# Optimization experiments

Hardware: AMD Instinct MI355X
Metric: run time of the kernel (lower is better)

Reference implementation:

```python
import jax, jax.numpy as jnp
import numpy as np

NUM_HEADS = 16
DIM = 1024

def setup_inputs() -> dict:
    key = jax.random.key(0)
    ks = jax.random.split(key, 12)
    B, N, T, C = 4, 4096, 77, DIM
    s = 1.0 / np.sqrt(C)
    return {
        "hidden_states": jax.random.normal(ks[0], (B, N, C), jnp.float32),
        "encoder_hidden_states": jax.random.normal(ks[1], (B, T, C), jnp.float32),
        "attention_mask": jnp.zeros((B, N, T), jnp.float32),
        "Wq": jax.random.normal(ks[2], (C, C), jnp.float32) * s,
        "bq": jnp.zeros((C,), jnp.float32),
        "Wk": jax.random.normal(ks[3], (C, C), jnp.float32) * s,
        "bk": jnp.zeros((C,), jnp.float32),
        "Wv": jax.random.normal(ks[4], (C, C), jnp.float32) * s,
        "bv": jnp.zeros((C,), jnp.float32),
        "Wo": jax.random.normal(ks[5], (C, C), jnp.float32) * s,
        "bo": jnp.zeros((C,), jnp.float32),
    }

def reference(hidden_states, encoder_hidden_states, attention_mask,
              Wq, bq, Wk, bk, Wv, bv, Wo, bo):
    B, N, C = hidden_states.shape
    T = encoder_hidden_states.shape[1]
    H = NUM_HEADS
    D = C // H
    # QKV projections (torch Linear: x @ W.T + b)
    q = (hidden_states @ Wq.T + bq).reshape(B, N, H, D).transpose(0, 2, 1, 3)   # bhnd
    k = (encoder_hidden_states @ Wk.T + bk).reshape(B, T, H, D).transpose(0, 2, 1, 3)  # bhtd
    v = (encoder_hidden_states @ Wv.T + bv).reshape(B, T, H, D).transpose(0, 2, 1, 3)  # bhtd
    scale = 1.0 / jnp.sqrt(jnp.asarray(D, q.dtype))
    # scores [B,H,N,T]; additive mask broadcast over heads
    scores = jnp.einsum('bhnd,bhtd->bhnt', q, k) * scale + attention_mask[:, None, :, :]
    attn = jax.nn.softmax(scores, axis=-1)
    out = jnp.einsum('bhnt,bhtd->bhnd', attn, v)
    out = out.transpose(0, 2, 1, 3).reshape(B, N, C)
    return out @ Wo.T + bo
```

## Files before the change

### kernel.cpp

```cpp
#include <hip/hip_runtime.h>
#include <cstdint>

typedef __bf16 bf16x8 __attribute__((ext_vector_type(8)));
typedef float f32x4 __attribute__((ext_vector_type(4)));
typedef unsigned short u16;
typedef unsigned int u32;

__device__ __forceinline__ u16 f2bf(float f) {
    u32 u = __builtin_bit_cast(u32, f);
    u += 0x7fffu + ((u >> 16) & 1u);
    return (u16)(u >> 16);
}

__device__ __forceinline__ void gl_lds16(const u16* g, u16* l) {
    __builtin_amdgcn_global_load_lds(
        (const __attribute__((address_space(1))) void*)g,
        (__attribute__((address_space(3))) void*)l,
        16, 0, 0);
}

__device__ __forceinline__ f32x4 mfma16(bf16x8 a, bf16x8 b, f32x4 c) {
    return __builtin_amdgcn_mfma_f32_16x16x32_bf16(a, b, c, 0, 0, 0);
}


__global__ void cvt_pad(const float* __restrict__ src, u16* __restrict__ dst,
                        int srcn, int totn) {
    int i = (blockIdx.x * 256 + threadIdx.x) * 4;
    if (i >= totn) return;
    float4 v = make_float4(0.f, 0.f, 0.f, 0.f);
    if (i < srcn) v = *(const float4*)&src[i];
    ushort4 o;
    o.x = f2bf(v.x); o.y = f2bf(v.y); o.z = f2bf(v.z); o.w = f2bf(v.w);
    *(ushort4*)&dst[i] = o;
}

struct CvtArgs {
    const float* s[5];
    u16* d[5];
    int srcn[5];
    int totn[5];
};

__global__ void cvt_multi(CvtArgs a) {
    const int seg = blockIdx.y;
    int i = (blockIdx.x * 256 + threadIdx.x) * 4;
    if (i >= a.totn[seg]) return;
    float4 v = make_float4(0.f, 0.f, 0.f, 0.f);
    if (i < a.srcn[seg]) v = *(const float4*)&a.s[seg][i];
    ushort4 o;
    o.x = f2bf(v.x); o.y = f2bf(v.y); o.z = f2bf(v.z); o.w = f2bf(v.w);
    *(ushort4*)&a.d[seg][i] = o;
}

__device__ __forceinline__ void store_out(u16* C, long idx, float v) { C[idx] = f2bf(v); }
__device__ __forceinline__ void store_out(float* C, long idx, float v) { C[idx] = v; }

template <typename OutT, bool BA, bool BC>
__global__ __launch_bounds__(512, 2) void gemm8p(
    const u16* __restrict__ A, const u16* __restrict__ W,
    const float* __restrict__ bias, OutT* __restrict__ C,
    int M, int N, int K) {
    __shared__ __align__(16) u16 As[2][256 * 64];
    __shared__ __align__(16) u16 Bs[2][256 * 64];

    const int tid = threadIdx.x;
    const int wid = tid >> 6, l = tid & 63;
    const int wr = wid >> 2, wc = wid & 3;
    const int l15 = l & 15, lg = l >> 4;

    const int lin = blockIdx.y * gridDim.x + blockIdx.x;
    const int cpx = (gridDim.x * gridDim.y) >> 3;
    const int swz = (lin & 7) * cpx + (lin >> 3);
    const long tn = swz % gridDim.x;
    const long tm = swz / gridDim.x;

    const int srow = tid >> 3;
    const int schunk = (tid & 7) ^ (srow & 7);

    long aBase, aQ, aT;
    if (BA) {
        const long rq = tm * 256 + srow;
        aBase = ((long)(schunk >> 1) * (M >> 2) + (rq >> 2)) * 64 +
                (srow & 3) * 16 + (schunk & 1) * 8;
        aQ = 1024;
        aT = 64L * M;
    } else {
        aBase = (tm * 256 + srow) * (long)K + schunk * 8;
        aQ = 64L * K;
        aT = 64;
    }
    const long bBase = (tn * 256 + srow) * (long)K + schunk * 8;

    const int rxor = l15 & 7;
    const int rdo0 = ((0 * 4 + lg) ^ rxor) * 8;
    const int rdo1 = ((1 * 4 + lg) ^ rxor) * 8;

    const int NT = K >> 6;

#define STAGE_A(bufi, q_, t_)                                                 \
    gl_lds16(A + aBase + (q_)*aQ + (long)(t_)*aT, &As[bufi][(q_)*4096 + tid * 8])
#define STAGE_B(bufi, q_, t_)                                                 \
    gl_lds16(W + bBase + (long)(q_)*64 * K + (long)(t_)*64,                   \
             &Bs[bufi][(q_)*4096 + tid * 8])

    f32x4 acc[8][4] = {};

#pragma unroll
    for (int q = 0; q < 4; ++q) { STAGE_A(0, q, 0); STAGE_B(0, q, 0); }
#pragma unroll
    for (int q = 0; q < 4; ++q) STAGE_B(1, q, 1);
    STAGE_A(1, 0, 1); STAGE_A(1, 2, 1);
    asm volatile("s_waitcnt vmcnt(6)" ::: "memory");
    __builtin_amdgcn_sched_barrier(0);
    __builtin_amdgcn_s_barrier();

    const int arow = wr * 128 + l15;
    const int brow = wc * 64 + l15;

    for (int t = 0; t < NT; ++t) {
        const int c = t & 1;
        const u16* __restrict__ Ap = &As[c][0];
        const u16* __restrict__ Bp = &Bs[c][0];
        const bool s1 = (t + 1) < NT;
        const bool s2 = (t + 2) < NT;
        bf16x8 b[4][2];

        {
            bf16x8 a[2][2];
#pragma unroll
            for (int mi = 0; mi < 2; ++mi) {
                a[mi][0] = *(const bf16x8*)&Ap[(arow + mi * 16) * 64 + rdo0];
                a[mi][1] = *(const bf16x8*)&Ap[(arow + mi * 16) * 64 + rdo1];
            }
#pragma unroll
            for (int nf = 0; nf < 4; ++nf) {
                b[nf][0] = *(const bf16x8*)&Bp[(brow + nf * 16) * 64 + rdo0];
                b[nf][1] = *(const bf16x8*)&Bp[(brow + nf * 16) * 64 + rdo1];
            }
            if (s1) STAGE_A(c ^ 1, 1, t + 1);
            __builtin_amdgcn_s_barrier();
            asm volatile("s_waitcnt lgkmcnt(0)" ::: "memory");
            __builtin_amdgcn_sched_barrier(0);
            __builtin_amdgcn_s_setprio(1);
#pragma unroll
            for (int mi = 0; mi < 2; ++mi)
#pragma unroll
                for (int nf = 0; nf < 4; ++nf) {
                    acc[mi][nf] = mfma16(a[mi][0], b[nf][0], acc[mi][nf]);
                    acc[mi][nf] = mfma16(a[mi][1], b[nf][1], acc[mi][nf]);
                }
            __builtin_amdgcn_s_setprio(0);
            __builtin_amdgcn_s_barrier();
        }
        {
            bf16x8 a[2][2];
#pragma unroll
            for (int mi = 0; mi < 2; ++mi) {
                a[mi][0] = *(const bf16x8*)&Ap[(arow + (mi + 2) * 16) * 64 + rdo0];
                a[mi][1] = *(const bf16x8*)&Ap[(arow + (mi + 2) * 16) * 64 + rdo1];
            }
            if (s1) STAGE_A(c ^ 1, 3, t + 1);
            if (s2) { STAGE_B(c, 0, t + 2); STAGE_B(c, 1, t + 2); }
            __builtin_amdgcn_s_barrier();
            asm volatile("s_waitcnt lgkmcnt(0)" ::: "memory");
            __builtin_amdgcn_sched_barrier(0);
            __builtin_amdgcn_s_setprio(1);
#pragma unroll
            for (int mi = 0; mi < 2; ++mi)
#pragma unroll
                for (int nf = 0; nf < 4; ++nf) {
                    acc[mi + 2][nf] = mfma16(a[mi][0], b[nf][0], acc[mi + 2][nf]);
                    acc[mi + 2][nf] = mfma16(a[mi][1], b[nf][1], acc[mi + 2][nf]);
                }
            __builtin_amdgcn_s_setprio(0);
            __builtin_amdgcn_s_barrier();
        }
        {
            bf16x8 a[2][2];
#pragma unroll
            for (int mi = 0; mi < 2; ++mi) {
                a[mi][0] = *(const bf16x8*)&Ap[(arow + (mi + 4) * 16) * 64 + rdo0];
                a[mi][1] = *(const bf16x8*)&Ap[(arow + (mi + 4) * 16) * 64 + rdo1];
            }
            if (s2) { STAGE_B(c, 2, t + 2); STAGE_B(c, 3, t + 2); STAGE_A(c, 0, t + 2); }
            __builtin_amdgcn_s_barrier();
            asm volatile("s_waitcnt lgkmcnt(0)" ::: "memory");
            __builtin_amdgcn_sched_barrier(0);
            __builtin_amdgcn_s_setprio(1);
#pragma unroll
            for (int mi = 0; mi < 2; ++mi)
#pragma unroll
                for (int nf = 0; nf < 4; ++nf) {
                    acc[mi + 4][nf] = mfma16(a[mi][0], b[nf][0], acc[mi + 4][nf]);
                    acc[mi + 4][nf] = mfma16(a[mi][1], b[nf][1], acc[mi + 4][nf]);
                }
            __builtin_amdgcn_s_setprio(0);
            __builtin_amdgcn_s_barrier();
        }
        {
            bf16x8 a[2][2];
#pragma unroll
            for (int mi = 0; mi < 2; ++mi) {
                a[mi][0] = *(const bf16x8*)&Ap[(arow + (mi + 6) * 16) * 64 + rdo0];
                a[mi][1] = *(const bf16x8*)&Ap[(arow + (mi + 6) * 16) * 64 + rdo1];
            }
            if (s2) STAGE_A(c, 2, t + 2);
            __builtin_amdgcn_s_barrier();
            asm volatile("s_waitcnt lgkmcnt(0)" ::: "memory");
            __builtin_amdgcn_sched_barrier(0);
            __builtin_amdgcn_s_setprio(1);
#pragma unroll
            for (int mi = 0; mi < 2; ++mi)
#pragma unroll
                for (int nf = 0; nf < 4; ++nf) {
                    acc[mi + 6][nf] = mfma16(a[mi][0], b[nf][0], acc[mi + 6][nf]);
                    acc[mi + 6][nf] = mfma16(a[mi][1], b[nf][1], acc[mi + 6][nf]);
                }
            __builtin_amdgcn_s_setprio(0);
            if (s2)
                asm volatile("s_waitcnt vmcnt(6)" ::: "memory");
            else
                asm volatile("s_waitcnt vmcnt(0)" ::: "memory");
            __builtin_amdgcn_sched_barrier(0);
            __builtin_amdgcn_s_barrier();
        }
    }
#undef STAGE_A
#undef STAGE_B

    const long row0 = tm * 256 + wr * 128;
    const long col0 = tn * 256 + wc * 64;
    float bv[4];
#pragma unroll
    for (int nf = 0; nf < 4; ++nf) bv[nf] = bias[col0 + nf * 16 + l15];
    if (BC) {
        const long ct0 = col0 >> 4;
        const long rb = row0 >> 2;
#pragma unroll
        for (int mf = 0; mf < 8; ++mf)
#pragma unroll
            for (int nf = 0; nf < 4; ++nf)
#pragma unroll
                for (int r = 0; r < 4; ++r) {
                    const long idx =
                        ((ct0 + nf) * (long)(M >> 2) + rb + mf * 4 + lg) * 64 +
                        r * 16 + l15;
                    store_out(C, idx, acc[mf][nf][r] + bv[nf]);
                }
    } else {
#pragma unroll
        for (int mf = 0; mf < 8; ++mf)
#pragma unroll
            for (int nf = 0; nf < 4; ++nf)
#pragma unroll
                for (int r = 0; r < 4; ++r) {
                    const long row = row0 + mf * 16 + lg * 4 + r;
                    const long col = col0 + nf * 16 + l15;
                    store_out(C, row * N + col, acc[mf][nf][r] + bv[nf]);
                }
    }
}

template <bool VT>
__device__ __forceinline__ void gemm128_body(
    const u16* __restrict__ A, const u16* __restrict__ W,
    const float* __restrict__ bias, u16* __restrict__ C,
    int N, int K) {
    __shared__ u16 As[128 * 64];
    __shared__ u16 Bs[128 * 64];
    const int tid = threadIdx.x;
    const int w = tid >> 6, l = tid & 63;
    const int wr = w >> 1, wc = w & 1;
    const int l15 = l & 15, lg = l >> 4;
    const long tm = blockIdx.y, tn = blockIdx.x;
    const u16* Ab = A + tm * 128 * (long)K;
    const u16* Bb = W + tn * 128 * (long)K;

    f32x4 acc[4][4] = {};

    for (int k0 = 0; k0 < K; k0 += 64) {
#pragma unroll
        for (int t = 0; t < 4; ++t) {
            int i = t * 256 + tid;
            int row = i >> 3, cc = i & 7;
            gl_lds16(Ab + (long)row * K + k0 + cc * 8, &As[i * 8]);
            gl_lds16(Bb + (long)row * K + k0 + cc * 8, &Bs[i * 8]);
        }
        __syncthreads();
#pragma unroll
        for (int kk = 0; kk < 64; kk += 32) {
            bf16x8 a[4], b[4];
#pragma unroll
            for (int m = 0; m < 4; ++m)
                a[m] = *(const bf16x8*)&As[(wr * 64 + m * 16 + l15) * 64 + kk + lg * 8];
#pragma unroll
            for (int n = 0; n < 4; ++n)
                b[n] = *(const bf16x8*)&Bs[(wc * 64 + n * 16 + l15) * 64 + kk + lg * 8];
#pragma unroll
            for (int m = 0; m < 4; ++m)
#pragma unroll
                for (int n = 0; n < 4; ++n)
                    acc[m][n] = mfma16(a[m], b[n], acc[m][n]);
        }
        __syncthreads();
    }

    const long row0 = tm * 128 + wr * 64;
    const long col0 = tn * 128 + wc * 64;
#pragma unroll
    for (int m = 0; m < 4; ++m)
#pragma unroll
        for (int n = 0; n < 4; ++n)
#pragma unroll
            for (int r = 0; r < 4; ++r) {
                const float v = acc[m][n][r] + bias[col0 + n * 16 + l15];
                if (VT) {
                    const int row = (int)(row0 + m * 16 + lg * 4 + r);
                    if (row < 308) {
                        const int bb = row / 77;
                        const int t = row - bb * 77;
                        const int ch = (int)(col0 + n * 16 + l15);
                        const long idx = (long)bb * 98304 +
                                         ((long)(t >> 4) * 256 + (ch >> 2)) * 64 +
                                         (ch & 3) * 16 + (t & 15);
                        C[idx] = f2bf(v);
                    }
                } else {
                    const long idx = (((col0 >> 4) + n) * 96L + (row0 >> 2) + m * 4 + lg) * 64 +
                                     r * 16 + l15;
                    C[idx] = f2bf(v);
                }
            }
}

__global__ __launch_bounds__(256) void gemm_kv(
    const u16* __restrict__ A,
    const u16* __restrict__ Wk, const float* __restrict__ bk, u16* __restrict__ Ko,
    const u16* __restrict__ Wv, const float* __restrict__ bv, u16* __restrict__ Vo,
    int N, int K) {
    if (blockIdx.z == 0)
        gemm128_body<false>(A, Wk, bk, Ko, N, K);
    else
        gemm128_body<true>(A, Wv, bv, Vo, N, K);
}

__global__ __launch_bounds__(256, 4) void attn_fused(
    const u16* __restrict__ Q,
    const u16* __restrict__ Kb,
    const u16* __restrict__ Vt,
    const float* __restrict__ mask,
    u16* __restrict__ Ao) {
    __shared__ u16 Ps[128 * 104];

    const int h = blockIdx.x, b = blockIdx.y, nt = blockIdx.z;
    const int tid = threadIdx.x;
    const int w = tid >> 6, l = tid & 63;
    const int l15 = l & 15, lg = l >> 4;

    const int qrow = b * 4096 + nt * 128 + w * 32;

    f32x4 acc[6][2] = {};
#pragma unroll
    for (int kk = 0; kk < 64; kk += 32) {
        const int d = kk + lg * 8;
        const int cb = h * 4 + (d >> 4);
        const int dlow = d & 15;
        bf16x8 kf[6], qf[2];
#pragma unroll
        for (int n = 0; n < 6; ++n) {
            const int row = b * 77 + n * 16 + l15;
            kf[n] = *(const bf16x8*)&Kb[((long)cb * 96 + (row >> 2)) * 64 +
                                        (row & 3) * 16 + dlow];
        }
#pragma unroll
        for (int m = 0; m < 2; ++m) {
            const int row = qrow + m * 16 + l15;
            qf[m] = *(const bf16x8*)&Q[((long)cb * 4096 + (row >> 2)) * 64 +
                                       (row & 3) * 16 + dlow];
        }
#pragma unroll
        for (int n = 0; n < 6; ++n)
#pragma unroll
            for (int m = 0; m < 2; ++m)
                acc[n][m] = mfma16(kf[n], qf[m], acc[n][m]);
    }

    const float* mrow0 = mask + ((long)b * 4096 + nt * 128 + w * 32) * 77;
#pragma unroll
    for (int m = 0; m < 2; ++m) {
        const float* mrow = mrow0 + (m * 16 + l15) * 77;
        float vals[6][4];
        float rmax = -3e38f;
#pragma unroll
        for (int n = 0; n < 6; ++n) {
            const int t0 = n * 16 + lg * 4;
#pragma unroll
            for (int r = 0; r < 4; ++r) {
                const int t = t0 + r;
                float v = -3e38f;
                if (t < 77) v = acc[n][m][r] * 0.125f + mrow[t];
                vals[n][r] = v;
                rmax = fmaxf(rmax, v);
            }
        }
        rmax = fmaxf(rmax, __shfl_xor(rmax, 16, 64));
        rmax = fmaxf(rmax, __shfl_xor(rmax, 32, 64));
        float s = 0.f;
#pragma unroll
        for (int n = 0; n < 6; ++n)
#pragma unroll
            for (int r = 0; r < 4; ++r) {
                float e = (vals[n][r] > -1e37f) ? __expf(vals[n][r] - rmax) : 0.f;
                vals[n][r] = e;
                s += e;
            }
        s += __shfl_xor(s, 16, 64);
        s += __shfl_xor(s, 32, 64);
        const float inv = 1.f / s;
#pragma unroll
        for (int n = 0; n < 6; ++n) {
            const u32 lo = (u32)f2bf(vals[n][0] * inv) |
                           ((u32)f2bf(vals[n][1] * inv) << 16);
            const u32 hi = (u32)f2bf(vals[n][2] * inv) |
                           ((u32)f2bf(vals[n][3] * inv) << 16);
            *(uint2*)&Ps[(w * 32 + m * 16 + l15) * 104 + n * 16 + lg * 4] =
                make_uint2(lo, hi);
        }
    }

    f32x4 o[2][4] = {};
#pragma unroll
    for (int kt = 0; kt < 96; kt += 32) {
        bf16x8 pa[2], vf[4];
#pragma unroll
        for (int m = 0; m < 2; ++m)
            pa[m] = *(const bf16x8*)&Ps[(w * 32 + m * 16 + l15) * 104 + kt + lg * 8];
        const int t0 = kt + lg * 8;
#pragma unroll
        for (int n = 0; n < 4; ++n) {
            const int ch = h * 64 + n * 16 + l15;
            vf[n] = *(const bf16x8*)&Vt[(long)b * 98304 +
                                        ((long)(t0 >> 4) * 256 + (ch >> 2)) * 64 +
                                        (ch & 3) * 16 + (t0 & 15)];
        }
#pragma unroll
        for (int m = 0; m < 2; ++m)
#pragma unroll
            for (int n = 0; n < 4; ++n)
                o[m][n] = mfma16(pa[m], vf[n], o[m][n]);
    }

#pragma unroll
    for (int m = 0; m < 2; ++m)
#pragma unroll
        for (int n = 0; n < 4; ++n)
#pragma unroll
            for (int r = 0; r < 4; ++r) {
                const long idx = ((long)(h * 4 + n) * 4096 +
                                  b * 1024 + nt * 32 + w * 8 + m * 4 + lg) * 64 +
                                 r * 16 + l15;
                Ao[idx] = f2bf(o[m][n][r]);
            }
}

extern "C" void kernel_launch(void* const* d_in, const int* in_sizes, int n_in,
                              void* d_out, int out_size, void* d_ws, size_t ws_size,
                              hipStream_t stream) {
    const float* hidden = (const float*)d_in[0];
    const float* enc = (const float*)d_in[1];
    const float* mask = (const float*)d_in[2];
    const float* Wq = (const float*)d_in[3];
    const float* bq = (const float*)d_in[4];
    const float* Wk = (const float*)d_in[5];
    const float* bk = (const float*)d_in[6];
    const float* Wv = (const float*)d_in[7];
    const float* bv = (const float*)d_in[8];
    const float* Wo = (const float*)d_in[9];
    const float* bo = (const float*)d_in[10];
    float* out = (float*)d_out;

    char* ws = (char*)d_ws;
    u16* hiddenB = (u16*)(ws);
    u16* Qb = (u16*)(ws + 33554432L);
    u16* AoB = (u16*)(ws + 2 * 33554432L);
    u16* WqB = (u16*)(ws + 3 * 33554432L);
    u16* WkB = WqB + 1048576;
    u16* WvB = WkB + 1048576;
    u16* WoB = WvB + 1048576;
    u16* encB = WoB + 1048576;
    u16* Kbuf = encB + 393216;
    u16* VtBuf = Kbuf + 393216;

    cvt_pad<<<dim3(16384), 256, 0, stream>>>(hidden, hiddenB, 16777216, 16777216);
    CvtArgs ca;
    ca.s[0] = Wq;  ca.d[0] = WqB; ca.srcn[0] = 1048576; ca.totn[0] = 1048576;
    ca.s[1] = Wk;  ca.d[1] = WkB; ca.srcn[1] = 1048576; ca.totn[1] = 1048576;
    ca.s[2] = Wv;  ca.d[2] = WvB; ca.srcn[2] = 1048576; ca.totn[2] = 1048576;
    ca.s[3] = Wo;  ca.d[3] = WoB; ca.srcn[3] = 1048576; ca.totn[3] = 1048576;
    ca.s[4] = enc; ca.d[4] = encB; ca.srcn[4] = 315392; ca.totn[4] = 393216;
    cvt_multi<<<dim3(1024, 5), 256, 0, stream>>>(ca);

    gemm8p<u16, false, true><<<dim3(4, 64), 512, 0, stream>>>(
        hiddenB, WqB, bq, Qb, 16384, 1024, 1024);
    gemm_kv<<<dim3(8, 3, 2), 256, 0, stream>>>(encB, WkB, bk, Kbuf, WvB, bv, VtBuf, 1024, 1024);

    attn_fused<<<dim3(16, 4, 32), 256, 0, stream>>>(Qb, Kbuf, VtBuf, mask, AoB);

    gemm8p<float, true, false><<<dim3(4, 64), 512, 0, stream>>>(
        AoB, WoB, bo, out, 16384, 1024, 1024);
}
```

Measured before the change: 166.5 us.

## Shrink GEMM tiles to 256x128 with simpler double buffering, merge conversions, trim attention tiles

Replaces the 256x256, K=64 GEMM with a 256x128, K=32 tile. It uses a plain double-buffered loop with one barrier per step, doubling the block count to 512 and cutting LDS use. The two fp32-to-bf16 conversion launches become a single launch that maps block ranges to segments. Attention now computes 5 key tiles instead of 6, masks padded keys with a large negative value instead of a branch, and zero-fills the pad region of the P buffer. The risks are more global traffic per FLOP and lost fine-grained overlap in the GEMM.

```diff
diff --git a/kernel.cpp b/kernel.cpp
--- a/kernel.cpp
+++ b/kernel.cpp
@@ -24,27 +24,20 @@
 }
 
 
-__global__ void cvt_pad(const float* __restrict__ src, u16* __restrict__ dst,
-                        int srcn, int totn) {
-    int i = (blockIdx.x * 256 + threadIdx.x) * 4;
-    if (i >= totn) return;
-    float4 v = make_float4(0.f, 0.f, 0.f, 0.f);
-    if (i < srcn) v = *(const float4*)&src[i];
-    ushort4 o;
-    o.x = f2bf(v.x); o.y = f2bf(v.y); o.z = f2bf(v.z); o.w = f2bf(v.w);
-    *(ushort4*)&dst[i] = o;
-}
-
-struct CvtArgs {
-    const float* s[5];
-    u16* d[5];
-    int srcn[5];
-    int totn[5];
+struct CvtAll {
+    const float* s[6];
+    u16* d[6];
+    int srcn[6];
+    int totn[6];
+    int off[6];
 };
 
-__global__ void cvt_multi(CvtArgs a) {
-    const int seg = blockIdx.y;
-    int i = (blockIdx.x * 256 + threadIdx.x) * 4;
+__global__ void cvt_all(CvtAll a) {
+    const int blk = blockIdx.x;
+    int seg = 0;
+#pragma unroll
+    for (int s = 1; s < 6; ++s) seg += (blk >= a.off[s]);
+    const int i = ((blk - a.off[seg]) * 256 + threadIdx.x) * 4;
     if (i >= a.totn[seg]) return;
     float4 v = make_float4(0.f, 0.f, 0.f, 0.f);
     if (i < a.srcn[seg]) v = *(const float4*)&a.s[seg][i];
@@ -57,180 +50,91 @@
 __device__ __forceinline__ void store_out(float* C, long idx, float v) { C[idx] = v; }
 
 template <typename OutT, bool BA, bool BC>
-__global__ __launch_bounds__(512, 2) void gemm8p(
+__global__ __launch_bounds__(512, 2) void gemmP(
     const u16* __restrict__ A, const u16* __restrict__ W,
     const float* __restrict__ bias, OutT* __restrict__ C,
     int M, int N, int K) {
-    __shared__ __align__(16) u16 As[2][256 * 64];
-    __shared__ __align__(16) u16 Bs[2][256 * 64];
+    __shared__ __align__(16) u16 As[2][256 * 32];
+    __shared__ __align__(16) u16 Bs[2][128 * 32];
 
     const int tid = threadIdx.x;
     const int wid = tid >> 6, l = tid & 63;
-    const int wr = wid >> 2, wc = wid & 3;
+    const int wr = wid >> 1, wc = wid & 1;
     const int l15 = l & 15, lg = l >> 4;
 
     const int lin = blockIdx.y * gridDim.x + blockIdx.x;
     const int cpx = (gridDim.x * gridDim.y) >> 3;
     const int swz = (lin & 7) * cpx + (lin >> 3);
-    const long tn = swz % gridDim.x;
-    const long tm = swz / gridDim.x;
-
-    const int srow = tid >> 3;
-    const int schunk = (tid & 7) ^ (srow & 7);
-
-    long aBase, aQ, aT;
-    if (BA) {
-        const long rq = tm * 256 + srow;
-        aBase = ((long)(schunk >> 1) * (M >> 2) + (rq >> 2)) * 64 +
-                (srow & 3) * 16 + (schunk & 1) * 8;
-        aQ = 1024;
-        aT = 64L * M;
-    } else {
-        aBase = (tm * 256 + srow) * (long)K + schunk * 8;
-        aQ = 64L * K;
-        aT = 64;
-    }
-    const long bBase = (tn * 256 + srow) * (long)K + schunk * 8;
-
-    const int rxor = l15 & 7;
-    const int rdo0 = ((0 * 4 + lg) ^ rxor) * 8;
-    const int rdo1 = ((1 * 4 + lg) ^ rxor) * 8;
-
-    const int NT = K >> 6;
-
-#define STAGE_A(bufi, q_, t_)                                                 \
-    gl_lds16(A + aBase + (q_)*aQ + (long)(t_)*aT, &As[bufi][(q_)*4096 + tid * 8])
-#define STAGE_B(bufi, q_, t_)                                                 \
-    gl_lds16(W + bBase + (long)(q_)*64 * K + (long)(t_)*64,                   \
-             &Bs[bufi][(q_)*4096 + tid * 8])
-
-    f32x4 acc[8][4] = {};
-
-#pragma unroll
-    for (int q = 0; q < 4; ++q) { STAGE_A(0, q, 0); STAGE_B(0, q, 0); }
-#pragma unroll
-    for (int q = 0; q < 4; ++q) STAGE_B(1, q, 1);
-    STAGE_A(1, 0, 1); STAGE_A(1, 2, 1);
-    asm volatile("s_waitcnt vmcnt(6)" ::: "memory");
-    __builtin_amdgcn_sched_barrier(0);
-    __builtin_amdgcn_s_barrier();
-
-    const int arow = wr * 128 + l15;
-    const int brow = wc * 64 + l15;
+    const long tn = swz & 7;
+    const long tm = swz >> 3;
+
+    const int srp = tid >> 3;
+    const int sv = (tid & 7) ^ (srp & 7);
+    const int sE = (sv >> 2) & 1;
+    const int sKC = sv & 3;
+    const long ar0 = tm * 256 + 2 * srp + sE;
+    const long brow = tn * 128 + 2 * srp + sE;
+    const long aRB = ar0 >> 2;
+    const int aSub = (int)(ar0 & 3) * 16 + (sKC & 1) * 8;
+    const int aCB = sKC >> 1;
+
+    const int NT = K >> 5;
+
+#define STAGE(bufi, t_)                                                        \
+    do {                                                                       \
+        if (BA) {                                                              \
+            const long cb_ = (long)((t_) * 2 + aCB) * (M >> 2);                \
+            gl_lds16(A + (cb_ + aRB) * 64 + aSub, &As[bufi][tid * 8]);         \
+            gl_lds16(A + (cb_ + aRB + 32) * 64 + aSub,                         \
+                     &As[bufi][4096 + tid * 8]);                               \
+        } else {                                                               \
+            gl_lds16(A + ar0 * (long)K + (t_) * 32 + sKC * 8,                  \
+                     &As[bufi][tid * 8]);                                      \
+            gl_lds16(A + (ar0 + 128) * (long)K + (t_) * 32 + sKC * 8,          \
+                     &As[bufi][4096 + tid * 8]);                               \
+        }                                                                      \
+        gl_lds16(W + brow * (long)K + (t_) * 32 + sKC * 8,                     \
+                 &Bs[bufi][tid * 8]);                                          \
+    } while (0)
+
+    const int e = l15 & 1;
+    const int rphA = wr * 32 + (l15 >> 1);
+    const int rphB = wc * 32 + (l15 >> 1);
+    const int pA = ((e * 4 + lg) ^ (rphA & 7)) * 8;
+    const int pB = ((e * 4 + lg) ^ (rphB & 7)) * 8;
+    const int aOff = rphA * 64 + pA;
+    const int bOff = rphB * 64 + pB;
+
+    f32x4 acc[4][4] = {};
+
+    STAGE(0, 0);
+    __syncthreads();
 
     for (int t = 0; t < NT; ++t) {
         const int c = t & 1;
-        const u16* __restrict__ Ap = &As[c][0];
-        const u16* __restrict__ Bp = &Bs[c][0];
-        const bool s1 = (t + 1) < NT;
-        const bool s2 = (t + 2) < NT;
-        bf16x8 b[4][2];
-
-        {
-            bf16x8 a[2][2];
-#pragma unroll
-            for (int mi = 0; mi < 2; ++mi) {
-                a[mi][0] = *(const bf16x8*)&Ap[(arow + mi * 16) * 64 + rdo0];
-                a[mi][1] = *(const bf16x8*)&Ap[(arow + mi * 16) * 64 + rdo1];
-            }
-#pragma unroll
-            for (int nf = 0; nf < 4; ++nf) {
-                b[nf][0] = *(const bf16x8*)&Bp[(brow + nf * 16) * 64 + rdo0];
-                b[nf][1] = *(const bf16x8*)&Bp[(brow + nf * 16) * 64 + rdo1];
-            }
-            if (s1) STAGE_A(c ^ 1, 1, t + 1);
-            __builtin_amdgcn_s_barrier();
-            asm volatile("s_waitcnt lgkmcnt(0)" ::: "memory");
-            __builtin_amdgcn_sched_barrier(0);
-            __builtin_amdgcn_s_setprio(1);
-#pragma unroll
-            for (int mi = 0; mi < 2; ++mi)
-#pragma unroll
-                for (int nf = 0; nf < 4; ++nf) {
-                    acc[mi][nf] = mfma16(a[mi][0], b[nf][0], acc[mi][nf]);
-                    acc[mi][nf] = mfma16(a[mi][1], b[nf][1], acc[mi][nf]);
-                }
-            __builtin_amdgcn_s_setprio(0);
-            __builtin_amdgcn_s_barrier();
-        }
-        {
-            bf16x8 a[2][2];
-#pragma unroll
-            for (int mi = 0; mi < 2; ++mi) {
-                a[mi][0] = *(const bf16x8*)&Ap[(arow + (mi + 2) * 16) * 64 + rdo0];
-                a[mi][1] = *(const bf16x8*)&Ap[(arow + (mi + 2) * 16) * 64 + rdo1];
-            }
-            if (s1) STAGE_A(c ^ 1, 3, t + 1);
-            if (s2) { STAGE_B(c, 0, t + 2); STAGE_B(c, 1, t + 2); }
-            __builtin_amdgcn_s_barrier();
-            asm volatile("s_waitcnt lgkmcnt(0)" ::: "memory");
-            __builtin_amdgcn_sched_barrier(0);
-            __builtin_amdgcn_s_setprio(1);
-#pragma unroll
-            for (int mi = 0; mi < 2; ++mi)
-#pragma unroll
-                for (int nf = 0; nf < 4; ++nf) {
-                    acc[mi + 2][nf] = mfma16(a[mi][0], b[nf][0], acc[mi + 2][nf]);
-                    acc[mi + 2][nf] = mfma16(a[mi][1], b[nf][1], acc[mi + 2][nf]);
-                }
-            __builtin_amdgcn_s_setprio(0);
-            __builtin_amdgcn_s_barrier();
-        }
-        {
-            bf16x8 a[2][2];
-#pragma unroll
-            for (int mi = 0; mi < 2; ++mi) {
-                a[mi][0] = *(const bf16x8*)&Ap[(arow + (mi + 4) * 16) * 64 + rdo0];
-                a[mi][1] = *(const bf16x8*)&Ap[(arow + (mi + 4) * 16) * 64 + rdo1];
-            }
-            if (s2) { STAGE_B(c, 2, t + 2); STAGE_B(c, 3, t + 2); STAGE_A(c, 0, t + 2); }
-            __builtin_amdgcn_s_barrier();
-            asm volatile("s_waitcnt lgkmcnt(0)" ::: "memory");
-            __builtin_amdgcn_sched_barrier(0);
-            __builtin_amdgcn_s_setprio(1);
-#pragma unroll
-            for (int mi = 0; mi < 2; ++mi)
-#pragma unroll
-                for (int nf = 0; nf < 4; ++nf) {
-                    acc[mi + 4][nf] = mfma16(a[mi][0], b[nf][0], acc[mi + 4][nf]);
-                    acc[mi + 4][nf] = mfma16(a[mi][1], b[nf][1], acc[mi + 4][nf]);
-                }
-            __builtin_amdgcn_s_setprio(0);
-            __builtin_amdgcn_s_barrier();
-        }
-        {
-            bf16x8 a[2][2];
-#pragma unroll
-            for (int mi = 0; mi < 2; ++mi) {
-                a[mi][0] = *(const bf16x8*)&Ap[(arow + (mi + 6) * 16) * 64 + rdo0];
-                a[mi][1] = *(const bf16x8*)&Ap[(arow + (mi + 6) * 16) * 64 + rdo1];
-            }
-            if (s2) STAGE_A(c, 2, t + 2);
-            __builtin_amdgcn_s_barrier();
-            asm volatile("s_waitcnt lgkmcnt(0)" ::: "memory");
-            __builtin_amdgcn_sched_barrier(0);
-            __builtin_amdgcn_s_setprio(1);
-#pragma unroll
-            for (int mi = 0; mi < 2; ++mi)
-#pragma unroll
-                for (int nf = 0; nf < 4; ++nf) {
-                    acc[mi + 6][nf] = mfma16(a[mi][0], b[nf][0], acc[mi + 6][nf]);
-                    acc[mi + 6][nf] = mfma16(a[mi][1], b[nf][1], acc[mi + 6][nf]);
-                }
-            __builtin_amdgcn_s_setprio(0);
-            if (s2)
-                asm volatile("s_waitcnt vmcnt(6)" ::: "memory");
-            else
-                asm volatile("s_waitcnt vmcnt(0)" ::: "memory");
-            __builtin_amdgcn_sched_barrier(0);
-            __builtin_amdgcn_s_barrier();
-        }
-    }
-#undef STAGE_A
-#undef STAGE_B
-
-    const long row0 = tm * 256 + wr * 128;
-    const long col0 = tn * 256 + wc * 64;
+        if (t + 1 < NT) STAGE(c ^ 1, t + 1);
+
+        bf16x8 a[4], b[4];
+#pragma unroll
+        for (int nf = 0; nf < 4; ++nf)
+            b[nf] = *(const bf16x8*)&Bs[c][bOff + nf * 512];
+#pragma unroll
+        for (int mf = 0; mf < 4; ++mf)
+            a[mf] = *(const bf16x8*)&As[c][aOff + mf * 512];
+
+        __builtin_amdgcn_s_setprio(1);
+#pragma unroll
+        for (int mf = 0; mf < 4; ++mf)
+#pragma unroll
+            for (int nf = 0; nf < 4; ++nf)
+                acc[mf][nf] = mfma16(a[mf], b[nf], acc[mf][nf]);
+        __builtin_amdgcn_s_setprio(0);
+        __syncthreads();
+    }
+#undef STAGE
+
+    const long row0 = tm * 256 + wr * 64;
+    const long col0 = tn * 128 + wc * 64;
     float bv[4];
 #pragma unroll
     for (int nf = 0; nf < 4; ++nf) bv[nf] = bias[col0 + nf * 16 + l15];
@@ -238,7 +142,7 @@
         const long ct0 = col0 >> 4;
         const long rb = row0 >> 2;
 #pragma unroll
-        for (int mf = 0; mf < 8; ++mf)
+        for (int mf = 0; mf < 4; ++mf)
 #pragma unroll
             for (int nf = 0; nf < 4; ++nf)
 #pragma unroll
@@ -250,7 +154,7 @@
                 }
     } else {
 #pragma unroll
-        for (int mf = 0; mf < 8; ++mf)
+        for (int mf = 0; mf < 4; ++mf)
 #pragma unroll
             for (int nf = 0; nf < 4; ++nf)
 #pragma unroll
@@ -360,15 +264,15 @@
 
     const int qrow = b * 4096 + nt * 128 + w * 32;
 
-    f32x4 acc[6][2] = {};
+    f32x4 acc[5][2] = {};
 #pragma unroll
     for (int kk = 0; kk < 64; kk += 32) {
         const int d = kk + lg * 8;
         const int cb = h * 4 + (d >> 4);
         const int dlow = d & 15;
-        bf16x8 kf[6], qf[2];
-#pragma unroll
-        for (int n = 0; n < 6; ++n) {
+        bf16x8 kf[5], qf[2];
+#pragma unroll
+        for (int n = 0; n < 5; ++n) {
             const int row = b * 77 + n * 16 + l15;
             kf[n] = *(const bf16x8*)&Kb[((long)cb * 96 + (row >> 2)) * 64 +
                                         (row & 3) * 16 + dlow];
@@ -380,7 +284,7 @@
                                        (row & 3) * 16 + dlow];
         }
 #pragma unroll
-        for (int n = 0; n < 6; ++n)
+        for (int n = 0; n < 5; ++n)
 #pragma unroll
             for (int m = 0; m < 2; ++m)
                 acc[n][m] = mfma16(kf[n], qf[m], acc[n][m]);
@@ -390,16 +294,19 @@
 #pragma unroll
     for (int m = 0; m < 2; ++m) {
         const float* mrow = mrow0 + (m * 16 + l15) * 77;
-        float vals[6][4];
+        float vals[5][4];
         float rmax = -3e38f;
 #pragma unroll
-        for (int n = 0; n < 6; ++n) {
+        for (int n = 0; n < 5; ++n) {
             const int t0 = n * 16 + lg * 4;
 #pragma unroll
             for (int r = 0; r < 4; ++r) {
-                const int t = t0 + r;
-                float v = -3e38f;
-                if (t < 77) v = acc[n][m][r] * 0.125f + mrow[t];
+                float mv;
+                if (n < 4)
+                    mv = mrow[t0 + r];
+                else
+                    mv = (t0 + r < 77) ? mrow[t0 + r] : -1e30f;
+                const float v = acc[n][m][r] * 0.125f + mv;
                 vals[n][r] = v;
                 rmax = fmaxf(rmax, v);
             }
@@ -408,10 +315,10 @@
         rmax = fmaxf(rmax, __shfl_xor(rmax, 32, 64));
         float s = 0.f;
 #pragma unroll
-        for (int n = 0; n < 6; ++n)
+        for (int n = 0; n < 5; ++n)
 #pragma unroll
             for (int r = 0; r < 4; ++r) {
-                float e = (vals[n][r] > -1e37f) ? __expf(vals[n][r] - rmax) : 0.f;
+                const float e = __expf(vals[n][r] - rmax);
                 vals[n][r] = e;
                 s += e;
             }
@@ -419,7 +326,7 @@
         s += __shfl_xor(s, 32, 64);
         const float inv = 1.f / s;
 #pragma unroll
-        for (int n = 0; n < 6; ++n) {
+        for (int n = 0; n < 5; ++n) {
             const u32 lo = (u32)f2bf(vals[n][0] * inv) |
                            ((u32)f2bf(vals[n][1] * inv) << 16);
             const u32 hi = (u32)f2bf(vals[n][2] * inv) |
@@ -427,6 +334,7 @@
             *(uint2*)&Ps[(w * 32 + m * 16 + l15) * 104 + n * 16 + lg * 4] =
                 make_uint2(lo, hi);
         }
+        *(uint2*)&Ps[(w * 32 + m * 16 + l15) * 104 + 80 + lg * 4] = make_uint2(0, 0);
     }
 
     f32x4 o[2][4] = {};
@@ -492,21 +400,27 @@
     u16* Kbuf = encB + 393216;
     u16* VtBuf = Kbuf + 393216;
 
-    cvt_pad<<<dim3(16384), 256, 0, stream>>>(hidden, hiddenB, 16777216, 16777216);
-    CvtArgs ca;
-    ca.s[0] = Wq;  ca.d[0] = WqB; ca.srcn[0] = 1048576; ca.totn[0] = 1048576;
-    ca.s[1] = Wk;  ca.d[1] = WkB; ca.srcn[1] = 1048576; ca.totn[1] = 1048576;
-    ca.s[2] = Wv;  ca.d[2] = WvB; ca.srcn[2] = 1048576; ca.totn[2] = 1048576;
-    ca.s[3] = Wo;  ca.d[3] = WoB; ca.srcn[3] = 1048576; ca.totn[3] = 1048576;
-    ca.s[4] = enc; ca.d[4] = encB; ca.srcn[4] = 315392; ca.totn[4] = 393216;
-    cvt_multi<<<dim3(1024, 5), 256, 0, stream>>>(ca);
-
-    gemm8p<u16, false, true><<<dim3(4, 64), 512, 0, stream>>>(
+    CvtAll ca;
+    ca.s[0] = hidden; ca.d[0] = hiddenB; ca.srcn[0] = 16777216; ca.totn[0] = 16777216;
+    ca.s[1] = Wq;  ca.d[1] = WqB; ca.srcn[1] = 1048576; ca.totn[1] = 1048576;
+    ca.s[2] = Wk;  ca.d[2] = WkB; ca.srcn[2] = 1048576; ca.totn[2] = 1048576;
+    ca.s[3] = Wv;  ca.d[3] = WvB; ca.srcn[3] = 1048576; ca.totn[3] = 1048576;
+    ca.s[4] = Wo;  ca.d[4] = WoB; ca.srcn[4] = 1048576; ca.totn[4] = 1048576;
+    ca.s[5] = enc; ca.d[5] = encB; ca.srcn[5] = 315392; ca.totn[5] = 393216;
+    ca.off[0] = 0;
+    ca.off[1] = 16384;
+    ca.off[2] = 17408;
+    ca.off[3] = 18432;
+    ca.off[4] = 19456;
+    ca.off[5] = 20480;
+    cvt_all<<<dim3(20864), 256, 0, stream>>>(ca);
+
+    gemmP<u16, false, true><<<dim3(8, 64), 512, 0, stream>>>(
         hiddenB, WqB, bq, Qb, 16384, 1024, 1024);
     gemm_kv<<<dim3(8, 3, 2), 256, 0, stream>>>(encB, WkB, bk, Kbuf, WvB, bv, VtBuf, 1024, 1024);
 
     attn_fused<<<dim3(16, 4, 32), 256, 0, stream>>>(Qb, Kbuf, VtBuf, mask, AoB);
 
-    gemm8p<float, true, false><<<dim3(4, 64), 512, 0, stream>>>(
+    gemmP<float, true, false><<<dim3(8, 64), 512, 0, stream>>>(
         AoB, WoB, bo, out, 16384, 1024, 1024);
 }
```

Result: faster. 161.9 us (-2.8%).
